# Optimization experiments

Measured on AMD Instinct MI355X. Metric: run time of the kernel, lower is better.

Reference implementation:

```python
import jax, jax.numpy as jnp
import numpy as np

EPS = 1e-5  # batch-norm epsilon


def subm_conv(feat, nbrs, W):
    # feat: [N, Cin], nbrs: [N, K] int indices into feat (rulebook), W: [K, Cin, Cout]
    gathered = feat[nbrs]                      # [N, K, Cin]  irregular gather
    return jnp.einsum('nkc,kcd->nd', gathered, W)


def batch_norm(f, gamma, beta):
    # training-mode BN over active sites (scn.BatchNormalization semantics)
    mean = jnp.mean(f, axis=0)
    var = jnp.var(f, axis=0)
    return (f - mean) * jax.lax.rsqrt(var + EPS) * gamma + beta


def setup_inputs() -> dict:
    key = jax.random.key(0)
    k1, k2, k3, k4 = jax.random.split(key, 4)
    N, K, C = 300000, 9, 64
    scale = 1.0 / np.sqrt(K * C)
    return {
        'x': jax.random.normal(k1, (N, C), dtype=jnp.float32),
        'nbrs': jax.random.randint(k2, (N, K), 0, N, dtype=jnp.int32),
        'W1': jax.random.normal(k3, (K, C, C), dtype=jnp.float32) * scale,
        'gamma1': jnp.ones((C,), jnp.float32),
        'beta1': jnp.zeros((C,), jnp.float32),
        'W2': jax.random.normal(k4, (K, C, C), dtype=jnp.float32) * scale,
        'gamma2': jnp.ones((C,), jnp.float32),
        'beta2': jnp.zeros((C,), jnp.float32),
    }


def reference(x, nbrs, W1, gamma1, beta1, W2, gamma2, beta2):
    residual = x
    out = subm_conv(x, nbrs, W1)                       # conv1 (no bias)
    out = jax.nn.relu(batch_norm(out, gamma1, beta1))  # BatchNormReLU
    out = subm_conv(out, nbrs, W2)                     # conv2 (no bias)
    out = batch_norm(out, gamma2, beta2)               # BatchNormalization
    out = jax.nn.relu(out + residual)                  # AddTable + ReLU
    return out
```

## Files before the change

### kernel.cpp

```cpp
#include <hip/hip_runtime.h>

#define NROWS 300000
#define NBLK ((NROWS + 63) / 64)

typedef float f32x4 __attribute__((ext_vector_type(4)));
typedef short s16x8 __attribute__((ext_vector_type(8)));
typedef unsigned short u16x8 __attribute__((ext_vector_type(8)));
typedef unsigned short u16x4 __attribute__((ext_vector_type(4)));

__device__ __forceinline__ float bf2f(unsigned short u) {
    return __uint_as_float(((unsigned)u) << 16);
}
__device__ __forceinline__ unsigned short f2bf(float f) {
    unsigned u = __float_as_uint(f);
    u += 0x7FFFu + ((u >> 16) & 1u);
    return (unsigned short)(u >> 16);
}

__device__ __forceinline__ void load_lds16(const void* g, void* lds) {
    __builtin_amdgcn_global_load_lds(
        (const __attribute__((address_space(1))) void*)g,
        (__attribute__((address_space(3))) void*)lds, 16, 0, 0);
}

__global__ __launch_bounds__(256) void x2bf(const float* __restrict__ x,
                                            unsigned short* __restrict__ xb) {
    const int NQ = NROWS * 8;
    for (int i = blockIdx.x * 256 + threadIdx.x; i < NQ; i += gridDim.x * 256) {
        const float4 v0 = *(const float4*)(x + (size_t)i * 8);
        const float4 v1 = *(const float4*)(x + (size_t)i * 8 + 4);
        u16x8 o;
        o[0] = f2bf(v0.x); o[1] = f2bf(v0.y); o[2] = f2bf(v0.z); o[3] = f2bf(v0.w);
        o[4] = f2bf(v1.x); o[5] = f2bf(v1.y); o[6] = f2bf(v1.z); o[7] = f2bf(v1.w);
        *(u16x8*)(xb + (size_t)i * 8) = o;
    }
}

__global__ __launch_bounds__(256) void w_prep(const float* __restrict__ W1,
                                              const float* __restrict__ W2,
                                              unsigned short* __restrict__ WT1,
                                              unsigned short* __restrict__ WT2) {
    const int i = blockIdx.x * 256 + threadIdx.x;
    if (i < 9 * 4096) {
        const int k = i >> 12, cc = (i >> 6) & 63, d = i & 63;
        const int o = k * 4096 + d * 64 + cc;
        WT1[o] = f2bf(W1[i]);
        WT2[o] = f2bf(W2[i]);
    }
}

__global__ __launch_bounds__(256) void conv_mfma(const unsigned short* __restrict__ xb,
                                                 const int* __restrict__ nbrs,
                                                 const unsigned short* __restrict__ WT,
                                                 unsigned short* __restrict__ outb) {
    __shared__ __align__(1024) char lds_raw[4 * 18432];

    const int tid = threadIdx.x;
    const int l = tid & 63;
    const int w = tid >> 6;
    const int lr = l & 15;
    const int kg = l >> 4;
    const int c00 = kg * 8;

    const int rowbase = blockIdx.x * 64 + w * 16;

    const int rsub = l >> 3;
    const int b16 = ((l & 7) ^ ((rsub & 1) << 2)) << 4;
    const int rA = min(rowbase + rsub, NROWS - 1);
    const int rB = min(rowbase + 8 + rsub, NROWS - 1);

    int nbA[9], nbB[9];
#pragma unroll
    for (int k = 0; k < 9; ++k) {
        nbA[k] = nbrs[rA * 9 + k];
        nbB[k] = nbrs[rB * 9 + k];
    }

    char* wbase = lds_raw + w * 18432;
    const char* xbc = (const char*)xb;
#pragma unroll
    for (int k = 0; k < 9; ++k) {
        load_lds16(xbc + (size_t)nbA[k] * 128 + b16, wbase + k * 2048);
        load_lds16(xbc + (size_t)nbB[k] * 128 + b16, wbase + k * 2048 + 1024);
    }
    asm volatile("s_waitcnt vmcnt(0)" ::: "memory");
    __builtin_amdgcn_sched_barrier(0);

    f32x4 acc[4];
#pragma unroll
    for (int d = 0; d < 4; ++d) {
        acc[d][0] = 0.f; acc[d][1] = 0.f; acc[d][2] = 0.f; acc[d][3] = 0.f;
    }

    const int swz = (lr & 1) << 6;
#pragma unroll
    for (int k = 0; k < 9; ++k) {
        const char* tk = wbase + k * 2048 + (lr >> 3) * 1024 + (lr & 7) * 128;
        const s16x8 a0 = *(const s16x8*)(tk + ((c00 * 2) ^ swz));
        const s16x8 a1 = *(const s16x8*)(tk + ((64 + c00 * 2) ^ swz));
        const unsigned short* wp = WT + k * 4096 + lr * 64 + c00;
#pragma unroll
        for (int dj = 0; dj < 4; ++dj) {
            const s16x8 b0 = *(const s16x8*)(wp + dj * 1024);
            const s16x8 b1 = *(const s16x8*)(wp + dj * 1024 + 32);
            acc[dj] = __builtin_amdgcn_mfma_f32_16x16x32_bf16(a0, b0, acc[dj], 0, 0, 0);
            acc[dj] = __builtin_amdgcn_mfma_f32_16x16x32_bf16(a1, b1, acc[dj], 0, 0, 0);
        }
    }

    const int orow0 = rowbase + kg * 4;
#pragma unroll
    for (int dj = 0; dj < 4; ++dj) {
#pragma unroll
        for (int r = 0; r < 4; ++r) {
            const int orow = orow0 + r;
            if (orow < NROWS) outb[(size_t)orow * 64 + dj * 16 + lr] = f2bf(acc[dj][r]);
        }
    }
}

__global__ __launch_bounds__(256) void bn_stats(const unsigned short* __restrict__ fb,
                                                float* __restrict__ S) {
    const int t = threadIdx.x;
    const int c4 = (t & 15) * 4;
    const int rg = t >> 4;
    float s0 = 0, s1 = 0, s2 = 0, s3 = 0, q0 = 0, q1 = 0, q2 = 0, q3 = 0;
    for (int r = blockIdx.x * 16 + rg; r < NROWS; r += gridDim.x * 16) {
        const u16x4 v = *(const u16x4*)(fb + (size_t)r * 64 + c4);
        const float f0 = bf2f(v[0]), f1 = bf2f(v[1]), f2 = bf2f(v[2]), f3 = bf2f(v[3]);
        s0 += f0; s1 += f1; s2 += f2; s3 += f3;
        q0 += f0 * f0; q1 += f1 * f1; q2 += f2 * f2; q3 += f3 * f3;
    }
    __shared__ float red[16][64];
    red[rg][c4 + 0] = s0; red[rg][c4 + 1] = s1; red[rg][c4 + 2] = s2; red[rg][c4 + 3] = s3;
    __syncthreads();
    if (t < 64) {
        float a = 0;
#pragma unroll
        for (int i = 0; i < 16; ++i) a += red[i][t];
        atomicAdd(&S[t], a);
    }
    __syncthreads();
    red[rg][c4 + 0] = q0; red[rg][c4 + 1] = q1; red[rg][c4 + 2] = q2; red[rg][c4 + 3] = q3;
    __syncthreads();
    if (t < 64) {
        float a = 0;
#pragma unroll
        for (int i = 0; i < 16; ++i) a += red[i][t];
        atomicAdd(&S[64 + t], a);
    }
}

__global__ void bn_finalize(const float* __restrict__ S, const float* __restrict__ gamma,
                            const float* __restrict__ beta, float* __restrict__ sb) {
    const int c = threadIdx.x;
    if (c < 64) {
        const float mean = S[c] * (1.0f / NROWS);
        const float var = S[64 + c] * (1.0f / NROWS) - mean * mean;
        const float sc = gamma[c] * rsqrtf(var + 1e-5f);
        sb[c] = sc;
        sb[64 + c] = beta[c] - mean * sc;
    }
}

__global__ __launch_bounds__(256) void bn_apply(unsigned short* __restrict__ fb,
                                                const float* __restrict__ sb) {
    const int NQ = NROWS * 8;
    for (int i = blockIdx.x * 256 + threadIdx.x; i < NQ; i += gridDim.x * 256) {
        const int c8 = (i & 7) * 8;
        u16x8 v = *(const u16x8*)(fb + (size_t)i * 8);
        u16x8 o;
#pragma unroll
        for (int j = 0; j < 8; ++j) {
            const float f = fmaxf(bf2f(v[j]) * sb[c8 + j] + sb[64 + c8 + j], 0.f);
            o[j] = f2bf(f);
        }
        *(u16x8*)(fb + (size_t)i * 8) = o;
    }
}

__global__ __launch_bounds__(256) void final_out(const unsigned short* __restrict__ o2,
                                                 const float* __restrict__ x,
                                                 const float* __restrict__ sb,
                                                 float* __restrict__ out) {
    const int NQ = NROWS * 16;
    for (int i = blockIdx.x * 256 + threadIdx.x; i < NQ; i += gridDim.x * 256) {
        const int c4 = (i & 15) * 4;
        const u16x4 v = *(const u16x4*)(o2 + (size_t)i * 4);
        const float4 xv = *(const float4*)(x + (size_t)i * 4);
        const float4 s = *(const float4*)(sb + c4);
        const float4 b = *(const float4*)(sb + 64 + c4);
        float4 o;
        o.x = fmaxf(bf2f(v[0]) * s.x + b.x + xv.x, 0.f);
        o.y = fmaxf(bf2f(v[1]) * s.y + b.y + xv.y, 0.f);
        o.z = fmaxf(bf2f(v[2]) * s.z + b.z + xv.z, 0.f);
        o.w = fmaxf(bf2f(v[3]) * s.w + b.w + xv.w, 0.f);
        *(float4*)(out + (size_t)i * 4) = o;
    }
}

extern "C" void kernel_launch(void* const* d_in, const int* in_sizes, int n_in,
                              void* d_out, int out_size, void* d_ws, size_t ws_size,
                              hipStream_t stream) {
    const float* x      = (const float*)d_in[0];
    const int*   nbrs   = (const int*)d_in[1];
    const float* W1     = (const float*)d_in[2];
    const float* gamma1 = (const float*)d_in[3];
    const float* beta1  = (const float*)d_in[4];
    const float* W2     = (const float*)d_in[5];
    const float* gamma2 = (const float*)d_in[6];
    const float* beta2  = (const float*)d_in[7];
    float* out = (float*)d_out;

    char* ws = (char*)d_ws;
    unsigned short* out2b = (unsigned short*)ws;
    unsigned short* WT1   = (unsigned short*)(ws + 38400000);
    unsigned short* WT2   = (unsigned short*)(ws + 38400000 + 73728);
    float* Sa  = (float*)(ws + 38400000 + 147456);
    float* Sb  = Sa + 128;
    float* sb1 = Sa + 256;
    float* sb2 = Sa + 384;
    unsigned short* out1b = (unsigned short*)d_out;
    unsigned short* xb    = (unsigned short*)d_out + 19200000;

    hipMemsetAsync(Sa, 0, 256 * sizeof(float), stream);
    x2bf<<<2048, 256, 0, stream>>>(x, xb);
    w_prep<<<144, 256, 0, stream>>>(W1, W2, WT1, WT2);
    conv_mfma<<<NBLK, 256, 0, stream>>>(xb, nbrs, WT1, out1b);
    bn_stats<<<1024, 256, 0, stream>>>(out1b, Sa);
    bn_finalize<<<1, 64, 0, stream>>>(Sa, gamma1, beta1, sb1);
    bn_apply<<<2048, 256, 0, stream>>>(out1b, sb1);
    conv_mfma<<<NBLK, 256, 0, stream>>>(out1b, nbrs, WT2, out2b);
    bn_stats<<<1024, 256, 0, stream>>>(out2b, Sb);
    bn_finalize<<<1, 64, 0, stream>>>(Sb, gamma2, beta2, sb2);
    final_out<<<2048, 256, 0, stream>>>(out2b, x, sb2, out);
}
```

Before: 528.9 us.

## Fuse BN statistics into conv epilogue and BN-apply+ReLU into conv2 gather

```diff
diff --git a/kernel.cpp b/kernel.cpp
--- a/kernel.cpp
+++ b/kernel.cpp
@@ -27,11 +27,11 @@
                                             unsigned short* __restrict__ xb) {
     const int NQ = NROWS * 8;
     for (int i = blockIdx.x * 256 + threadIdx.x; i < NQ; i += gridDim.x * 256) {
-        const float4 v0 = *(const float4*)(x + (size_t)i * 8);
-        const float4 v1 = *(const float4*)(x + (size_t)i * 8 + 4);
+        const f32x4 v0 = *(const f32x4*)(x + (size_t)i * 8);
+        const f32x4 v1 = *(const f32x4*)(x + (size_t)i * 8 + 4);
         u16x8 o;
-        o[0] = f2bf(v0.x); o[1] = f2bf(v0.y); o[2] = f2bf(v0.z); o[3] = f2bf(v0.w);
-        o[4] = f2bf(v1.x); o[5] = f2bf(v1.y); o[6] = f2bf(v1.z); o[7] = f2bf(v1.w);
+        o[0] = f2bf(v0[0]); o[1] = f2bf(v0[1]); o[2] = f2bf(v0[2]); o[3] = f2bf(v0[3]);
+        o[4] = f2bf(v1[0]); o[5] = f2bf(v1[1]); o[6] = f2bf(v1[2]); o[7] = f2bf(v1[3]);
         *(u16x8*)(xb + (size_t)i * 8) = o;
     }
 }
@@ -49,11 +49,16 @@
     }
 }
 
+template <int CONV>
 __global__ __launch_bounds__(256) void conv_mfma(const unsigned short* __restrict__ xb,
                                                  const int* __restrict__ nbrs,
                                                  const unsigned short* __restrict__ WT,
-                                                 unsigned short* __restrict__ outb) {
+                                                 const float* __restrict__ sb,
+                                                 unsigned short* __restrict__ outb,
+                                                 float* __restrict__ S) {
     __shared__ __align__(1024) char lds_raw[4 * 18432];
+    __shared__ float SSum[4][64];
+    __shared__ float SSq[4][64];
 
     const int tid = threadIdx.x;
     const int l = tid & 63;
@@ -64,6 +69,15 @@
 
     const int rowbase = blockIdx.x * 64 + w * 16;
 
+    float s0r[8], b0r[8], s1r[8], b1r[8];
+    if (CONV == 2) {
+#pragma unroll
+        for (int j = 0; j < 8; ++j) {
+            s0r[j] = sb[c00 + j];       b0r[j] = sb[64 + c00 + j];
+            s1r[j] = sb[32 + c00 + j];  b1r[j] = sb[96 + c00 + j];
+        }
+    }
+
     const int rsub = l >> 3;
     const int b16 = ((l & 7) ^ ((rsub & 1) << 2)) << 4;
     const int rA = min(rowbase + rsub, NROWS - 1);
@@ -96,8 +110,17 @@
 #pragma unroll
     for (int k = 0; k < 9; ++k) {
         const char* tk = wbase + k * 2048 + (lr >> 3) * 1024 + (lr & 7) * 128;
-        const s16x8 a0 = *(const s16x8*)(tk + ((c00 * 2) ^ swz));
-        const s16x8 a1 = *(const s16x8*)(tk + ((64 + c00 * 2) ^ swz));
+        s16x8 a0 = *(const s16x8*)(tk + ((c00 * 2) ^ swz));
+        s16x8 a1 = *(const s16x8*)(tk + ((64 + c00 * 2) ^ swz));
+        if (CONV == 2) {
+#pragma unroll
+            for (int j = 0; j < 8; ++j) {
+                const float f0 = fmaxf(bf2f((unsigned short)a0[j]) * s0r[j] + b0r[j], 0.f);
+                const float f1 = fmaxf(bf2f((unsigned short)a1[j]) * s1r[j] + b1r[j], 0.f);
+                a0[j] = (short)f2bf(f0);
+                a1[j] = (short)f2bf(f1);
+            }
+        }
         const unsigned short* wp = WT + k * 4096 + lr * 64 + c00;
 #pragma unroll
         for (int dj = 0; dj < 4; ++dj) {
@@ -111,43 +134,30 @@
     const int orow0 = rowbase + kg * 4;
 #pragma unroll
     for (int dj = 0; dj < 4; ++dj) {
+        float sm = 0.f, sq = 0.f;
 #pragma unroll
         for (int r = 0; r < 4; ++r) {
             const int orow = orow0 + r;
-            if (orow < NROWS) outb[(size_t)orow * 64 + dj * 16 + lr] = f2bf(acc[dj][r]);
-        }
-    }
-}
-
-__global__ __launch_bounds__(256) void bn_stats(const unsigned short* __restrict__ fb,
-                                                float* __restrict__ S) {
-    const int t = threadIdx.x;
-    const int c4 = (t & 15) * 4;
-    const int rg = t >> 4;
-    float s0 = 0, s1 = 0, s2 = 0, s3 = 0, q0 = 0, q1 = 0, q2 = 0, q3 = 0;
-    for (int r = blockIdx.x * 16 + rg; r < NROWS; r += gridDim.x * 16) {
-        const u16x4 v = *(const u16x4*)(fb + (size_t)r * 64 + c4);
-        const float f0 = bf2f(v[0]), f1 = bf2f(v[1]), f2 = bf2f(v[2]), f3 = bf2f(v[3]);
-        s0 += f0; s1 += f1; s2 += f2; s3 += f3;
-        q0 += f0 * f0; q1 += f1 * f1; q2 += f2 * f2; q3 += f3 * f3;
-    }
-    __shared__ float red[16][64];
-    red[rg][c4 + 0] = s0; red[rg][c4 + 1] = s1; red[rg][c4 + 2] = s2; red[rg][c4 + 3] = s3;
+            if (orow < NROWS) {
+                const float v = acc[dj][r];
+                const unsigned short bv = f2bf(v);
+                if (CONV == 2)
+                    __builtin_nontemporal_store(bv, &outb[(size_t)orow * 64 + dj * 16 + lr]);
+                else
+                    outb[(size_t)orow * 64 + dj * 16 + lr] = bv;
+                sm += v; sq += v * v;
+            }
+        }
+        sm += __shfl_xor(sm, 16); sm += __shfl_xor(sm, 32);
+        sq += __shfl_xor(sq, 16); sq += __shfl_xor(sq, 32);
+        if (kg == 0) { SSum[w][dj * 16 + lr] = sm; SSq[w][dj * 16 + lr] = sq; }
+    }
     __syncthreads();
-    if (t < 64) {
-        float a = 0;
-#pragma unroll
-        for (int i = 0; i < 16; ++i) a += red[i][t];
-        atomicAdd(&S[t], a);
-    }
-    __syncthreads();
-    red[rg][c4 + 0] = q0; red[rg][c4 + 1] = q1; red[rg][c4 + 2] = q2; red[rg][c4 + 3] = q3;
-    __syncthreads();
-    if (t < 64) {
-        float a = 0;
-#pragma unroll
-        for (int i = 0; i < 16; ++i) a += red[i][t];
-        atomicAdd(&S[64 + t], a);
+    if (tid < 64) {
+        const float sm = SSum[0][tid] + SSum[1][tid] + SSum[2][tid] + SSum[3][tid];
+        const float sq = SSq[0][tid] + SSq[1][tid] + SSq[2][tid] + SSq[3][tid];
+        atomicAdd(&S[tid], sm);
+        atomicAdd(&S[64 + tid], sq);
     }
 }
 
@@ -163,22 +173,6 @@
     }
 }
 
-__global__ __launch_bounds__(256) void bn_apply(unsigned short* __restrict__ fb,
-                                                const float* __restrict__ sb) {
-    const int NQ = NROWS * 8;
-    for (int i = blockIdx.x * 256 + threadIdx.x; i < NQ; i += gridDim.x * 256) {
-        const int c8 = (i & 7) * 8;
-        u16x8 v = *(const u16x8*)(fb + (size_t)i * 8);
-        u16x8 o;
-#pragma unroll
-        for (int j = 0; j < 8; ++j) {
-            const float f = fmaxf(bf2f(v[j]) * sb[c8 + j] + sb[64 + c8 + j], 0.f);
-            o[j] = f2bf(f);
-        }
-        *(u16x8*)(fb + (size_t)i * 8) = o;
-    }
-}
-
 __global__ __launch_bounds__(256) void final_out(const unsigned short* __restrict__ o2,
                                                  const float* __restrict__ x,
                                                  const float* __restrict__ sb,
@@ -186,16 +180,16 @@
     const int NQ = NROWS * 16;
     for (int i = blockIdx.x * 256 + threadIdx.x; i < NQ; i += gridDim.x * 256) {
         const int c4 = (i & 15) * 4;
-        const u16x4 v = *(const u16x4*)(o2 + (size_t)i * 4);
-        const float4 xv = *(const float4*)(x + (size_t)i * 4);
-        const float4 s = *(const float4*)(sb + c4);
-        const float4 b = *(const float4*)(sb + 64 + c4);
-        float4 o;
-        o.x = fmaxf(bf2f(v[0]) * s.x + b.x + xv.x, 0.f);
-        o.y = fmaxf(bf2f(v[1]) * s.y + b.y + xv.y, 0.f);
-        o.z = fmaxf(bf2f(v[2]) * s.z + b.z + xv.z, 0.f);
-        o.w = fmaxf(bf2f(v[3]) * s.w + b.w + xv.w, 0.f);
-        *(float4*)(out + (size_t)i * 4) = o;
+        const u16x4 v = __builtin_nontemporal_load((const u16x4*)(o2 + (size_t)i * 4));
+        const f32x4 xv = __builtin_nontemporal_load((const f32x4*)(x + (size_t)i * 4));
+        const f32x4 s = *(const f32x4*)(sb + c4);
+        const f32x4 b = *(const f32x4*)(sb + 64 + c4);
+        f32x4 o;
+        o[0] = fmaxf(bf2f(v[0]) * s[0] + b[0] + xv[0], 0.f);
+        o[1] = fmaxf(bf2f(v[1]) * s[1] + b[1] + xv[1], 0.f);
+        o[2] = fmaxf(bf2f(v[2]) * s[2] + b[2] + xv[2], 0.f);
+        o[3] = fmaxf(bf2f(v[3]) * s[3] + b[3] + xv[3], 0.f);
+        __builtin_nontemporal_store(o, (f32x4*)(out + (size_t)i * 4));
     }
 }
 
@@ -226,12 +220,9 @@
     hipMemsetAsync(Sa, 0, 256 * sizeof(float), stream);
     x2bf<<<2048, 256, 0, stream>>>(x, xb);
     w_prep<<<144, 256, 0, stream>>>(W1, W2, WT1, WT2);
-    conv_mfma<<<NBLK, 256, 0, stream>>>(xb, nbrs, WT1, out1b);
-    bn_stats<<<1024, 256, 0, stream>>>(out1b, Sa);
+    conv_mfma<1><<<NBLK, 256, 0, stream>>>(xb, nbrs, WT1, nullptr, out1b, Sa);
     bn_finalize<<<1, 64, 0, stream>>>(Sa, gamma1, beta1, sb1);
-    bn_apply<<<2048, 256, 0, stream>>>(out1b, sb1);
-    conv_mfma<<<NBLK, 256, 0, stream>>>(out1b, nbrs, WT2, out2b);
-    bn_stats<<<1024, 256, 0, stream>>>(out2b, Sb);
+    conv_mfma<2><<<NBLK, 256, 0, stream>>>(out1b, nbrs, WT2, sb1, out2b, Sb);
     bn_finalize<<<1, 64, 0, stream>>>(Sb, gamma2, beta2, sb2);
     final_out<<<2048, 256, 0, stream>>>(out2b, x, sb2, out);
 }
```

New measurement: 573.0 us. +8.3%, slower.
